# Kernel tuning notes

Hardware: AMD Instinct MI355X
Metric: run time of the kernel (lower is better)

Reference implementation:

```python
import jax, jax.numpy as jnp
import numpy as np

ALPHA = 0.2          # leaky relu negative slope
NEG_BIG = -9e15      # masking value used by the torch module


def setup_inputs() -> dict:
    key = jax.random.key(0)
    k1, k2, k3, k4, k5 = jax.random.split(key, 5)
    N, F_IN, F_OUT = 8192, 256, 64
    inputs = jax.random.normal(k1, (N, F_IN), dtype=jnp.float32)
    adj = jax.random.randint(k2, (N, N), 0, 2, dtype=jnp.int32)
    # xavier-normal-ish parameter init (scale is irrelevant for correctness testing)
    W = jax.random.normal(k3, (F_IN, F_OUT), dtype=jnp.float32) * np.sqrt(2.0 / (F_IN + F_OUT))
    a1 = jax.random.normal(k4, (F_OUT, 1), dtype=jnp.float32) * np.sqrt(2.0 / (F_OUT + 1))
    a2 = jax.random.normal(k5, (F_OUT, 1), dtype=jnp.float32) * np.sqrt(2.0 / (F_OUT + 1))
    return {"inputs": inputs, "adj": adj, "W": W, "a1": a1, "a2": a2}


def reference(inputs, adj, W, a1, a2):
    # h: [N, F_OUT]
    h = inputs @ W
    f1 = h @ a1                      # [N, 1]
    f2 = h @ a2                      # [N, 1]
    e = jax.nn.leaky_relu(f1 + f2.T, negative_slope=ALPHA)   # [N, N] broadcast additive score
    e = jnp.where(adj > 0, e, NEG_BIG)
    attention = jax.nn.softmax(e, axis=-1)                    # masked softmax over rows
    # dropout is identity in eval mode (training=False)
    h_prime = attention @ h                                   # [N, F_OUT]
    return jax.nn.elu(h_prime)                                # concat=True -> elu
```

## Files before the change

kernel.cpp:

```cpp
#include <hip/hip_runtime.h>
#include <hip/hip_bf16.h>

#define N     8192
#define FIN   256
#define FOUT  64
#define ALPHA 0.2f
#define KQ    16
#define JQ    (N / KQ)
#define JW    (JQ / 4)
#define NS    (JW / 32)

typedef __attribute__((ext_vector_type(8))) short bf16x8;
typedef __attribute__((ext_vector_type(4))) float f32x4;
typedef __attribute__((ext_vector_type(4))) int   i32x4;

static __device__ __forceinline__ unsigned short f2bf(float x) {
    union { float f; unsigned int u; } v; v.f = x;
    unsigned int r = v.u + 0x7FFFu + ((v.u >> 16) & 1u);
    return (unsigned short)(r >> 16);
}
static __device__ __forceinline__ float asf(unsigned int u) {
    union { unsigned int u; float f; } v; v.u = u; return v.f;
}
static __device__ __forceinline__ float wcalc(float f1v, float f2v, int a) {
    const float e = f1v + f2v;
    const float lr = fmaxf(e, ALPHA * e);
    const float w = __expf(lr);
    return (a > 0) ? w : 0.f;
}

__global__ __launch_bounds__(256) void k_h(
        const float* __restrict__ X, const float* __restrict__ W,
        const float* __restrict__ a1, const float* __restrict__ a2,
        unsigned short* __restrict__ hb,
        float* __restrict__ f1, float* __restrict__ f2) {
    const int lane = threadIdx.x & 63;
    const int wave = threadIdx.x >> 6;
    const int row0 = (blockIdx.x * 4 + wave) * 4;

    typedef __attribute__((ext_vector_type(4))) float f4;
    const f4* Xr[4];
    #pragma unroll
    for (int r = 0; r < 4; ++r)
        Xr[r] = (const f4*)(X + (size_t)(row0 + r) * FIN);

    float acc[4] = {0.f, 0.f, 0.f, 0.f};
    #pragma unroll 4
    for (int k4 = 0; k4 < FIN / 4; ++k4) {
        const float w0 = W[(k4 * 4 + 0) * FOUT + lane];
        const float w1 = W[(k4 * 4 + 1) * FOUT + lane];
        const float w2 = W[(k4 * 4 + 2) * FOUT + lane];
        const float w3 = W[(k4 * 4 + 3) * FOUT + lane];
        #pragma unroll
        for (int r = 0; r < 4; ++r) {
            const f4 xv = __builtin_nontemporal_load(&Xr[r][k4]);
            acc[r] = fmaf(xv.x, w0, acc[r]);
            acc[r] = fmaf(xv.y, w1, acc[r]);
            acc[r] = fmaf(xv.z, w2, acc[r]);
            acc[r] = fmaf(xv.w, w3, acc[r]);
        }
    }

    ushort4 hv;
    hv.x = f2bf(acc[0]); hv.y = f2bf(acc[1]);
    hv.z = f2bf(acc[2]); hv.w = f2bf(acc[3]);
    *(ushort4*)&hb[(size_t)(row0 >> 3) * 512 + lane * 8 + (row0 & 7)] = hv;

    const float a1v = a1[lane];
    const float a2v = a2[lane];
    #pragma unroll
    for (int r = 0; r < 4; ++r) {
        float p1 = acc[r] * a1v;
        float p2 = acc[r] * a2v;
        #pragma unroll
        for (int off = 32; off > 0; off >>= 1) {
            p1 += __shfl_down(p1, off);
            p2 += __shfl_down(p2, off);
        }
        if (lane == 0) { f1[row0 + r] = p1; f2[row0 + r] = p2; }
    }
}

__global__ __launch_bounds__(256, 6) void k_attn(
        const int* __restrict__ adj, const unsigned short* __restrict__ hb,
        const float* __restrict__ f1, const float* __restrict__ f2,
        float* __restrict__ part, float* __restrict__ pden) {
    __shared__ f32x4 red[2][256];
    __shared__ float dred[4][16];

    const int t    = threadIdx.x;
    const int lane = t & 63;
    const int wv   = t >> 6;
    const int bid  = blockIdx.x;
    const int rg   = bid >> 4;
    const int q    = bid & 15;
    const int i0   = rg * 16;
    const int r    = lane & 15;
    const int kg   = lane >> 4;

    const float f1v = f1[i0 + r];
    const int jw = q * JQ + wv * JW;
    const int* aptr = adj + (size_t)(i0 + r) * N + jw + kg * 8;
    const float* f2p = f2 + jw + kg * 8;
    const unsigned short* hbp = hb + (size_t)(jw >> 3) * 512 + kg * 512 + r * 8;

    i32x4 am[2 * NS];
    #pragma unroll
    for (int s = 0; s < NS; ++s) {
        am[2 * s]     = *(const i32x4*)(aptr + s * 32);
        am[2 * s + 1] = *(const i32x4*)(aptr + s * 32 + 4);
    }

    f32x4 acc[4];
    #pragma unroll
    for (int c = 0; c < 4; ++c) acc[c] = (f32x4){0.f, 0.f, 0.f, 0.f};
    float sacc = 0.f;

    #pragma unroll
    for (int s = 0; s < NS; ++s) {
        const unsigned short* hs = hbp + s * 2048;
        const bf16x8 b0 = *(const bf16x8*)(hs);
        const bf16x8 b1 = *(const bf16x8*)(hs + 128);
        const bf16x8 b2 = *(const bf16x8*)(hs + 256);
        const bf16x8 b3 = *(const bf16x8*)(hs + 384);

        const float4 fa = *(const float4*)(f2p + s * 32);
        const float4 fb = *(const float4*)(f2p + s * 32 + 4);
        const i32x4 a0 = am[2 * s];
        const i32x4 a1 = am[2 * s + 1];

        const float w0 = wcalc(f1v, fa.x, a0.x);
        const float w1 = wcalc(f1v, fa.y, a0.y);
        const float w2 = wcalc(f1v, fa.z, a0.z);
        const float w3 = wcalc(f1v, fa.w, a0.w);
        const float w4 = wcalc(f1v, fb.x, a1.x);
        const float w5 = wcalc(f1v, fb.y, a1.y);
        const float w6 = wcalc(f1v, fb.z, a1.z);
        const float w7 = wcalc(f1v, fb.w, a1.w);

        union { bf16x8 v; __hip_bfloat162 h2[4]; unsigned int u[4]; } af;
        af.h2[0] = __float22bfloat162_rn(make_float2(w0, w1));
        af.h2[1] = __float22bfloat162_rn(make_float2(w2, w3));
        af.h2[2] = __float22bfloat162_rn(make_float2(w4, w5));
        af.h2[3] = __float22bfloat162_rn(make_float2(w6, w7));

        float ds = 0.f;
        #pragma unroll
        for (int u = 0; u < 4; ++u)
            ds += asf(af.u[u] << 16) + asf(af.u[u] & 0xFFFF0000u);
        sacc += ds;

        acc[0] = __builtin_amdgcn_mfma_f32_16x16x32_bf16(af.v, b0, acc[0], 0, 0, 0);
        acc[1] = __builtin_amdgcn_mfma_f32_16x16x32_bf16(af.v, b1, acc[1], 0, 0, 0);
        acc[2] = __builtin_amdgcn_mfma_f32_16x16x32_bf16(af.v, b2, acc[2], 0, 0, 0);
        acc[3] = __builtin_amdgcn_mfma_f32_16x16x32_bf16(af.v, b3, acc[3], 0, 0, 0);
    }

    sacc += __shfl_xor(sacc, 16);
    sacc += __shfl_xor(sacc, 32);
    if (lane < 16) dred[wv][lane] = sacc;

    __syncthreads();
    if (wv >= 2) {
        #pragma unroll
        for (int cg = 0; cg < 4; ++cg) red[wv - 2][lane * 4 + cg] = acc[cg];
    }
    __syncthreads();
    if (wv < 2) {
        #pragma unroll
        for (int cg = 0; cg < 4; ++cg) acc[cg] += red[wv][lane * 4 + cg];
    }
    __syncthreads();
    if (wv == 1) {
        #pragma unroll
        for (int cg = 0; cg < 4; ++cg) red[0][lane * 4 + cg] = acc[cg];
    }
    __syncthreads();
    if (wv == 0) {
        #pragma unroll
        for (int cg = 0; cg < 4; ++cg) acc[cg] += red[0][lane * 4 + cg];
        #pragma unroll
        for (int cg = 0; cg < 4; ++cg)
            #pragma unroll
            for (int rr = 0; rr < 4; ++rr)
                __builtin_nontemporal_store(acc[cg][rr],
                    &part[(size_t)bid * 1024 + (kg * 4 + rr) * FOUT + cg * 16 + r]);
        if (lane < 16)
            __builtin_nontemporal_store(
                dred[0][lane] + dred[1][lane] + dred[2][lane] + dred[3][lane],
                &pden[bid * 16 + lane]);
    }
}

__global__ __launch_bounds__(256) void k_fin(
        const float* __restrict__ part, const float* __restrict__ pden,
        float* __restrict__ out) {
    const int rg = blockIdx.x;
    const int t  = threadIdx.x;
    const int r  = t >> 4;
    const int c4 = (t & 15) * 4;

    float vx = 0.f, vy = 0.f, vz = 0.f, vw = 0.f;
    float den = 0.f;
    #pragma unroll
    for (int p = 0; p < KQ; ++p) {
        const int blk = rg * KQ + p;
        const f32x4 pv = __builtin_nontemporal_load(
            (const f32x4*)&part[(size_t)blk * 1024 + r * FOUT + c4]);
        vx += pv.x; vy += pv.y; vz += pv.z; vw += pv.w;
        den += __builtin_nontemporal_load(&pden[blk * 16 + r]);
    }
    den = fmaxf(den, 1e-30f);
    const float inv = __fdividef(1.f, den);
    f32x4 o;
    const float h0 = vx * inv; o.x = (h0 > 0.f) ? h0 : (__expf(h0) - 1.f);
    const float h1 = vy * inv; o.y = (h1 > 0.f) ? h1 : (__expf(h1) - 1.f);
    const float h2 = vz * inv; o.z = (h2 > 0.f) ? h2 : (__expf(h2) - 1.f);
    const float h3 = vw * inv; o.w = (h3 > 0.f) ? h3 : (__expf(h3) - 1.f);
    __builtin_nontemporal_store(o,
        (f32x4*)&out[(size_t)(rg * 16 + r) * FOUT + c4]);
}

extern "C" void kernel_launch(void* const* d_in, const int* in_sizes, int n_in,
                              void* d_out, int out_size, void* d_ws, size_t ws_size,
                              hipStream_t stream) {
    const float* X   = (const float*)d_in[0];
    const int*   adj = (const int*)d_in[1];
    const float* W   = (const float*)d_in[2];
    const float* a1  = (const float*)d_in[3];
    const float* a2  = (const float*)d_in[4];
    float* out = (float*)d_out;

    unsigned short* hb = (unsigned short*)d_ws;
    float* f1   = (float*)((char*)d_ws + (size_t)FOUT * N * 2);
    float* f2   = f1 + N;
    float* part = f2 + N;
    float* pden = part + (size_t)(N / 16) * KQ * 1024;

    k_h   <<<N / 16, 256, 0, stream>>>(X, W, a1, a2, hb, f1, f2);
    k_attn<<<(N / 16) * KQ, 256, 0, stream>>>(adj, hb, f1, f2, part, pden);
    k_fin <<<N / 16, 256, 0, stream>>>(part, pden, out);
}
```

Baseline: 98.66 us.

## Stream adjacency tiles through double-buffered LDS with async global-to-LDS loads

Each attention block now covers a larger column range per row group, which halves the number of key partitions. The adjacency rows are staged in 256-column tiles into double-buffered shared memory using direct global-to-LDS loads with an XOR swizzle. The next tile is prefetched while the current one is consumed by the MFMA loop. This aims for more coalesced adj reads and overlap of memory with compute, at the cost of extra barriers, a less regular register-preload pattern, and a change in occupancy now that the launch-bounds occupancy hint is removed and shared memory use is larger.

```diff
diff --git a/kernel.cpp b/kernel.cpp
--- a/kernel.cpp
+++ b/kernel.cpp
@@ -5,10 +5,11 @@
 #define FIN   256
 #define FOUT  64
 #define ALPHA 0.2f
-#define KQ    16
+#define KQ    8
 #define JQ    (N / KQ)
-#define JW    (JQ / 4)
-#define NS    (JW / 32)
+#define TJ    256
+#define NTL   (JQ / TJ)
+#define NSW   2
 
 typedef __attribute__((ext_vector_type(8))) short bf16x8;
 typedef __attribute__((ext_vector_type(4))) float f32x4;
@@ -27,6 +28,15 @@
     const float lr = fmaxf(e, ALPHA * e);
     const float w = __expf(lr);
     return (a > 0) ? w : 0.f;
+}
+static __device__ __forceinline__ void gload_lds16(const int* g, int* l) {
+    __builtin_amdgcn_global_load_lds(
+        (const __attribute__((address_space(1))) void*)g,
+        (__attribute__((address_space(3))) void*)l,
+        16, 0, 0);
+}
+static __device__ __forceinline__ int rowperm(int row) {
+    return ((row << 1) | (row >> 3)) & 63;
 }
 
 __global__ __launch_bounds__(256) void k_h(
@@ -38,11 +48,10 @@
     const int wave = threadIdx.x >> 6;
     const int row0 = (blockIdx.x * 4 + wave) * 4;
 
-    typedef __attribute__((ext_vector_type(4))) float f4;
-    const f4* Xr[4];
+    const f32x4* Xr[4];
     #pragma unroll
     for (int r = 0; r < 4; ++r)
-        Xr[r] = (const f4*)(X + (size_t)(row0 + r) * FIN);
+        Xr[r] = (const f32x4*)(X + (size_t)(row0 + r) * FIN);
 
     float acc[4] = {0.f, 0.f, 0.f, 0.f};
     #pragma unroll 4
@@ -53,7 +62,7 @@
         const float w3 = W[(k4 * 4 + 3) * FOUT + lane];
         #pragma unroll
         for (int r = 0; r < 4; ++r) {
-            const f4 xv = __builtin_nontemporal_load(&Xr[r][k4]);
+            const f32x4 xv = __builtin_nontemporal_load(&Xr[r][k4]);
             acc[r] = fmaf(xv.x, w0, acc[r]);
             acc[r] = fmaf(xv.y, w1, acc[r]);
             acc[r] = fmaf(xv.z, w2, acc[r]);
@@ -81,10 +90,11 @@
     }
 }
 
-__global__ __launch_bounds__(256, 6) void k_attn(
+__global__ __launch_bounds__(256) void k_attn(
         const int* __restrict__ adj, const unsigned short* __restrict__ hb,
         const float* __restrict__ f1, const float* __restrict__ f2,
         float* __restrict__ part, float* __restrict__ pden) {
+    __shared__ int  tile[2][16][TJ];
     __shared__ f32x4 red[2][256];
     __shared__ float dred[4][16];
 
@@ -92,24 +102,15 @@
     const int lane = t & 63;
     const int wv   = t >> 6;
     const int bid  = blockIdx.x;
-    const int rg   = bid >> 4;
-    const int q    = bid & 15;
+    const int rg   = bid >> 3;
+    const int q    = bid & 7;
     const int i0   = rg * 16;
     const int r    = lane & 15;
     const int kg   = lane >> 4;
 
     const float f1v = f1[i0 + r];
-    const int jw = q * JQ + wv * JW;
-    const int* aptr = adj + (size_t)(i0 + r) * N + jw + kg * 8;
-    const float* f2p = f2 + jw + kg * 8;
-    const unsigned short* hbp = hb + (size_t)(jw >> 3) * 512 + kg * 512 + r * 8;
-
-    i32x4 am[2 * NS];
-    #pragma unroll
-    for (int s = 0; s < NS; ++s) {
-        am[2 * s]     = *(const i32x4*)(aptr + s * 32);
-        am[2 * s + 1] = *(const i32x4*)(aptr + s * 32 + 4);
-    }
+    const int jb = q * JQ;
+    const int pr = rowperm(r);
 
     f32x4 acc[4];
     #pragma unroll
@@ -117,43 +118,85 @@
     float sacc = 0.f;
 
     #pragma unroll
-    for (int s = 0; s < NS; ++s) {
-        const unsigned short* hs = hbp + s * 2048;
-        const bf16x8 b0 = *(const bf16x8*)(hs);
-        const bf16x8 b1 = *(const bf16x8*)(hs + 128);
-        const bf16x8 b2 = *(const bf16x8*)(hs + 256);
-        const bf16x8 b3 = *(const bf16x8*)(hs + 384);
-
-        const float4 fa = *(const float4*)(f2p + s * 32);
-        const float4 fb = *(const float4*)(f2p + s * 32 + 4);
-        const i32x4 a0 = am[2 * s];
-        const i32x4 a1 = am[2 * s + 1];
-
-        const float w0 = wcalc(f1v, fa.x, a0.x);
-        const float w1 = wcalc(f1v, fa.y, a0.y);
-        const float w2 = wcalc(f1v, fa.z, a0.z);
-        const float w3 = wcalc(f1v, fa.w, a0.w);
-        const float w4 = wcalc(f1v, fb.x, a1.x);
-        const float w5 = wcalc(f1v, fb.y, a1.y);
-        const float w6 = wcalc(f1v, fb.z, a1.z);
-        const float w7 = wcalc(f1v, fb.w, a1.w);
-
-        union { bf16x8 v; __hip_bfloat162 h2[4]; unsigned int u[4]; } af;
-        af.h2[0] = __float22bfloat162_rn(make_float2(w0, w1));
-        af.h2[1] = __float22bfloat162_rn(make_float2(w2, w3));
-        af.h2[2] = __float22bfloat162_rn(make_float2(w4, w5));
-        af.h2[3] = __float22bfloat162_rn(make_float2(w6, w7));
-
-        float ds = 0.f;
-        #pragma unroll
-        for (int u = 0; u < 4; ++u)
-            ds += asf(af.u[u] << 16) + asf(af.u[u] & 0xFFFF0000u);
-        sacc += ds;
-
-        acc[0] = __builtin_amdgcn_mfma_f32_16x16x32_bf16(af.v, b0, acc[0], 0, 0, 0);
-        acc[1] = __builtin_amdgcn_mfma_f32_16x16x32_bf16(af.v, b1, acc[1], 0, 0, 0);
-        acc[2] = __builtin_amdgcn_mfma_f32_16x16x32_bf16(af.v, b2, acc[2], 0, 0, 0);
-        acc[3] = __builtin_amdgcn_mfma_f32_16x16x32_bf16(af.v, b3, acc[3], 0, 0, 0);
+    for (int rr = 0; rr < 4; ++rr) {
+        const int row = wv * 4 + rr;
+        gload_lds16(adj + (size_t)(i0 + row) * N + jb + (lane ^ rowperm(row)) * 4,
+                    &tile[0][row][0]);
+    }
+    asm volatile("s_waitcnt vmcnt(0)" ::: "memory");
+    __builtin_amdgcn_s_barrier();
+
+    int buf = 0;
+    for (int tt = 0; tt < NTL; ++tt) {
+        const int jt = jb + tt * TJ;
+
+        bf16x8 bfr[NSW][4];
+        float4 fa[NSW], fb[NSW];
+        #pragma unroll
+        for (int ss = 0; ss < NSW; ++ss) {
+            const int s = wv * NSW + ss;
+            const float* f2s = f2 + jt + s * 32 + kg * 8;
+            fa[ss] = *(const float4*)(f2s);
+            fb[ss] = *(const float4*)(f2s + 4);
+            const unsigned short* hs =
+                hb + (size_t)((jt >> 3) + s * 4 + kg) * 512 + r * 8;
+            bfr[ss][0] = *(const bf16x8*)(hs);
+            bfr[ss][1] = *(const bf16x8*)(hs + 128);
+            bfr[ss][2] = *(const bf16x8*)(hs + 256);
+            bfr[ss][3] = *(const bf16x8*)(hs + 384);
+        }
+        __builtin_amdgcn_sched_barrier(0);
+
+        if (tt + 1 < NTL) {
+            #pragma unroll
+            for (int rr = 0; rr < 4; ++rr) {
+                const int row = wv * 4 + rr;
+                gload_lds16(adj + (size_t)(i0 + row) * N + jt + TJ
+                                + (lane ^ rowperm(row)) * 4,
+                            &tile[buf ^ 1][row][0]);
+            }
+            __builtin_amdgcn_sched_barrier(0);
+            asm volatile("s_waitcnt vmcnt(4)" ::: "memory");
+        } else {
+            asm volatile("s_waitcnt vmcnt(0)" ::: "memory");
+        }
+        __builtin_amdgcn_s_barrier();
+
+        #pragma unroll
+        for (int ss = 0; ss < NSW; ++ss) {
+            const int s = wv * NSW + ss;
+            const int g0 = s * 8 + kg * 2;
+            const i32x4 a0 = *(const i32x4*)&tile[buf][r][((g0 ^ pr) & 63) * 4];
+            const i32x4 a1 = *(const i32x4*)&tile[buf][r][(((g0 + 1) ^ pr) & 63) * 4];
+
+            const float w0 = wcalc(f1v, fa[ss].x, a0.x);
+            const float w1 = wcalc(f1v, fa[ss].y, a0.y);
+            const float w2 = wcalc(f1v, fa[ss].z, a0.z);
+            const float w3 = wcalc(f1v, fa[ss].w, a0.w);
+            const float w4 = wcalc(f1v, fb[ss].x, a1.x);
+            const float w5 = wcalc(f1v, fb[ss].y, a1.y);
+            const float w6 = wcalc(f1v, fb[ss].z, a1.z);
+            const float w7 = wcalc(f1v, fb[ss].w, a1.w);
+
+            union { bf16x8 v; __hip_bfloat162 h2[4]; unsigned int u[4]; } af;
+            af.h2[0] = __float22bfloat162_rn(make_float2(w0, w1));
+            af.h2[1] = __float22bfloat162_rn(make_float2(w2, w3));
+            af.h2[2] = __float22bfloat162_rn(make_float2(w4, w5));
+            af.h2[3] = __float22bfloat162_rn(make_float2(w6, w7));
+
+            float ds = 0.f;
+            #pragma unroll
+            for (int u = 0; u < 4; ++u)
+                ds += asf(af.u[u] << 16) + asf(af.u[u] & 0xFFFF0000u);
+            sacc += ds;
+
+            acc[0] = __builtin_amdgcn_mfma_f32_16x16x32_bf16(af.v, bfr[ss][0], acc[0], 0, 0, 0);
+            acc[1] = __builtin_amdgcn_mfma_f32_16x16x32_bf16(af.v, bfr[ss][1], acc[1], 0, 0, 0);
+            acc[2] = __builtin_amdgcn_mfma_f32_16x16x32_bf16(af.v, bfr[ss][2], acc[2], 0, 0, 0);
+            acc[3] = __builtin_amdgcn_mfma_f32_16x16x32_bf16(af.v, bfr[ss][3], acc[3], 0, 0, 0);
+        }
+        __builtin_amdgcn_s_barrier();
+        buf ^= 1;
     }
 
     sacc += __shfl_xor(sacc, 16);
```

New measurement: 86.75 us. 12.1% less time.
